# Kernel tuning notes

Measured on AMD Instinct MI355X. Metric: run time of the kernel, lower is better.

The kernel has to match this reference:

```python
import jax, jax.numpy as jnp
import numpy as np

B, N, D, H, MLP = 4, 1024, 1024, 16, 4096  # seq_len N must equal dim D; D = H * dim_head
DH = D // H
EPS = 1e-5


def layernorm(x, g, b):
    mu = jnp.mean(x, axis=-1, keepdims=True)
    var = jnp.var(x, axis=-1, keepdims=True)
    return (x - mu) * jax.lax.rsqrt(var + EPS) * g + b


def setup_inputs() -> dict:
    key = jax.random.key(0)
    ks = jax.random.split(key, 12)
    s = 0.02
    return {
        "x": jax.random.normal(ks[0], (B, N, D), jnp.float32),
        "enc_out": jax.random.normal(ks[1], (B, N, D), jnp.float32),
        # SelfAttention (heads=1, dim_head=D); weights stored (in, out) so we apply x @ W
        "sa_wq": jax.random.normal(ks[2], (D, D), jnp.float32) * s,
        "sa_wk": jax.random.normal(ks[3], (D, D), jnp.float32) * s,
        "sa_wv": jax.random.normal(ks[4], (D, D), jnp.float32) * s,
        "sa_g": jnp.ones((D,), jnp.float32),
        "sa_b": jnp.zeros((D,), jnp.float32),
        # CrossAttention
        "ca_wq": jax.random.normal(ks[5], (D, D), jnp.float32) * s,
        "ca_wk": jax.random.normal(ks[6], (D, D), jnp.float32) * s,
        "ca_wv": jax.random.normal(ks[7], (D, D), jnp.float32) * s,
        "ca_g": jnp.ones((D,), jnp.float32),
        "ca_b": jnp.zeros((D,), jnp.float32),
        # FeedForward
        "w1": jax.random.normal(ks[8], (D, MLP), jnp.float32) * s,
        "b1": jnp.zeros((MLP,), jnp.float32),
        "w2": jax.random.normal(ks[9], (MLP, D), jnp.float32) * s,
        "b2": jnp.zeros((D,), jnp.float32),
        "ff_g": jnp.ones((D,), jnp.float32),
        "ff_b": jnp.zeros((D,), jnp.float32),
    }


def reference(x, enc_out, sa_wq, sa_wk, sa_wv, sa_g, sa_b,
              ca_wq, ca_wk, ca_wv, ca_g, ca_b,
              w1, b1, w2, b2, ff_g, ff_b):
    b, n, d = x.shape
    # --- SelfAttention: heads=1, dim_head=dim -> scale = dim**-0.5 ---
    sa_scale = 1.0 / jnp.sqrt(jnp.asarray(d, x.dtype))
    q = x @ sa_wq
    k = x @ sa_wk
    v = x @ sa_wv
    dots = jnp.einsum('bid,bjd->bij', q, k) * sa_scale
    attn = jax.nn.softmax(dots, axis=-1)
    sa = jnp.einsum('bij,bjd->bid', attn, v)
    sa = layernorm(sa + x, sa_g, sa_b)

    # --- CrossAttention: Q . (K K^T) before softmax ---
    dh = d // H
    ca_scale = 1.0 / jnp.sqrt(jnp.asarray(dh, x.dtype))
    qc = sa @ ca_wq                                     # [b, n, d]; broadcast over heads
    kc = (enc_out @ ca_wk).reshape(b, n, H, dh).transpose(0, 2, 1, 3)  # [b, h, n, dh]
    vc = (enc_out @ ca_wv).reshape(b, n, H, dh).transpose(0, 2, 1, 3)
    kkt = jnp.einsum('bhid,bhjd->bhij', kc, kc) * ca_scale             # [b, h, n, n]
    dots = jnp.einsum('bid,bhjd->bhij', qc, kkt) * ca_scale            # q's d contracts kkt's last dim (n == d)
    attn = jax.nn.softmax(dots, axis=-1)
    out = jnp.einsum('bhij,bhjd->bhid', attn, vc)
    out = out.transpose(0, 2, 1, 3).reshape(b, n, d)
    ca = layernorm(out + enc_out, ca_g, ca_b)

    # --- FeedForward (dropout = identity in eval) ---
    h = jax.nn.gelu(ca @ w1 + b1, approximate=False) @ w2 + b2
    return layernorm(h + ca, ff_g, ff_b)
```

## Files before the change

kernel.cpp:

```cpp
#include <hip/hip_runtime.h>
#include <math.h>
#include <stdint.h>

typedef unsigned short u16;
typedef u16   u16x8 __attribute__((ext_vector_type(8)));
typedef __bf16 bf16x8 __attribute__((ext_vector_type(8)));
typedef float  f32x4 __attribute__((ext_vector_type(4)));

#define B_   4
#define N_   1024
#define D_   1024
#define MLP_ 4096

__device__ __forceinline__ float bf2f(u16 v) {
    unsigned u = ((unsigned)v) << 16;
    return __builtin_bit_cast(float, u);
}
__device__ __forceinline__ u16 f2bf(float f) {
    unsigned u = __builtin_bit_cast(unsigned, f);
    u += 0x7fff + ((u >> 16) & 1);
    return (u16)(u >> 16);
}
__device__ __forceinline__ bf16x8 ld8(const u16* p) {
    return __builtin_bit_cast(bf16x8, *(const u16x8*)p);
}
__device__ __forceinline__ void gll16(const u16* g, u16* l) {
    __builtin_amdgcn_global_load_lds(
        (const __attribute__((address_space(1))) unsigned int*)g,
        (__attribute__((address_space(3))) unsigned int*)l,
        16, 0, 0);
}

__global__ __launch_bounds__(256)
void prep_all(const float* __restrict__ x, const float* __restrict__ enc,
              u16* __restrict__ xB, u16* __restrict__ encB,
              const float* __restrict__ p0, const float* __restrict__ p1,
              const float* __restrict__ p2, const float* __restrict__ p3,
              const float* __restrict__ p4, const float* __restrict__ p5,
              u16* __restrict__ Wsa, u16* __restrict__ Wca)
{
    __shared__ u16 tile[32][33];
    int bid = blockIdx.x;
    if (bid < 4096) {
        const float* in = x; u16* out = xB;
        if (bid >= 2048) { in = enc; out = encB; bid -= 2048; }
        long i = (long)bid * 256 + threadIdx.x;
        f32x4 a = *(const f32x4*)&in[i * 8];
        f32x4 b = *(const f32x4*)&in[i * 8 + 4];
        u16x8 h;
        h[0] = f2bf(a[0]); h[1] = f2bf(a[1]); h[2] = f2bf(a[2]); h[3] = f2bf(a[3]);
        h[4] = f2bf(b[0]); h[5] = f2bf(b[1]); h[6] = f2bf(b[2]); h[7] = f2bf(b[3]);
        *(u16x8*)&out[i * 8] = h;
        return;
    }
    int sub = bid - 4096;
    const int z = sub >> 10;
    const int t2 = sub & 1023;
    const int bx = (t2 & 31) * 32, by = (t2 >> 5) * 32;
    const float* in = p0;
    if (z == 1) in = p1;
    else if (z == 2) in = p2;
    else if (z == 3) in = p3;
    else if (z == 4) in = p4;
    else if (z == 5) in = p5;
    u16* out = (z < 3) ? Wsa + (long)z * (1 << 20) : Wca + (long)(z - 3) * (1 << 20);
    const int tx = threadIdx.x & 31, ty = threadIdx.x >> 5;
#pragma unroll
    for (int i = ty; i < 32; i += 8)
        tile[i][tx] = f2bf(in[(long)(by + i) * 1024 + bx + tx]);
    __syncthreads();
#pragma unroll
    for (int i = ty; i < 32; i += 8)
        out[(long)(bx + i) * 1024 + by + tx] = tile[tx][i];
}

template<int TM, int TN, int SEL, int OUTF32, int BIAS, int GELU>
__global__ __launch_bounds__(256, (TM + TN >= 256) ? 3 : 4)
void gemm_a(const u16* __restrict__ A0, const u16* __restrict__ A1,
            const u16* __restrict__ B0, const u16* __restrict__ B1,
            void* __restrict__ C0v, void* __restrict__ C1v,
            const float* __restrict__ bias,
            float scale, int K,
            int lda, int ldb, int ldc,
            long sA, long sB, long sC)
{
    constexpr int MT = TM / 32, NT = TN / 32;
    __shared__ alignas(16) u16 As[2][TM * 32];
    __shared__ alignas(16) u16 Bs[2][TN * 32];
    int by = blockIdx.y, bz = blockIdx.z;
    const u16* A = A0; const u16* Bt = B0; char* Cp = (char*)C0v;
    if (SEL == 1) {
        int half = gridDim.y >> 1;
        if (by >= half) { A = A1; Bt = B1; Cp = (char*)C1v; by -= half; }
    }
    if (SEL == 2) {
        int half = gridDim.z >> 1;
        if (bz >= half) { A = A1; Bt = B1; Cp = (char*)C1v; bz -= half; }
    }
    A += bz * sA;  Bt += bz * sB;  Cp += bz * sC * (OUTF32 ? 4 : 2);
    const int m0 = blockIdx.x * TM, n0 = by * TN;
    const int t = threadIdx.x, lane = t & 63, w = t >> 6;
    const int wr = (w >> 1) * (TM / 2), wc = (w & 1) * (TN / 2);
    const int fr = lane & 15, fq = lane >> 4, fk = fq * 8;
    f32x4 acc[MT][NT] = {};

    const int r0a = t >> 2, c0a = (t & 3) * 8;
    auto stageA = [&](u16* dst, int k0) {
#pragma unroll
        for (int p = 0; p < TM / 64; p++)
            gll16(A + (long)(m0 + p * 64 + r0a) * lda + k0 + c0a, dst + p * 2048 + w * 512);
    };
    auto stageB = [&](u16* dst, int k0) {
#pragma unroll
        for (int p = 0; p < TN / 64; p++)
            gll16(Bt + (long)(n0 + p * 64 + r0a) * ldb + k0 + c0a, dst + p * 2048 + w * 512);
    };

    stageA(As[0], 0);
    stageB(Bs[0], 0);
    int cur = 0;
    for (int k0 = 0; k0 < K; k0 += 32) {
        __syncthreads();
        if (k0 + 32 < K) {
            stageA(As[cur ^ 1], k0 + 32);
            stageB(Bs[cur ^ 1], k0 + 32);
        }
        const u16* as = As[cur];
        const u16* bs = Bs[cur];
        bf16x8 af[MT], bfv[NT];
#pragma unroll
        for (int mt = 0; mt < MT; mt++) af [mt] = ld8(&as[(wr + mt * 16 + fr) * 32 + fk]);
#pragma unroll
        for (int nt = 0; nt < NT; nt++) bfv[nt] = ld8(&bs[(wc + nt * 16 + fr) * 32 + fk]);
#pragma unroll
        for (int mt = 0; mt < MT; mt++)
#pragma unroll
            for (int nt = 0; nt < NT; nt++)
                acc[mt][nt] = __builtin_amdgcn_mfma_f32_16x16x32_bf16(af[mt], bfv[nt], acc[mt][nt], 0, 0, 0);
        cur ^= 1;
    }

#pragma unroll
    for (int nt = 0; nt < NT; nt++) {
        const int col = n0 + wc + nt * 16 + fr;
        float bv = 0.f;
        if (BIAS) bv = bias[col];
#pragma unroll
        for (int mt = 0; mt < MT; mt++) {
            const int rbase = m0 + wr + mt * 16 + fq * 4;
#pragma unroll
            for (int r = 0; r < 4; r++) {
                float v = acc[mt][nt][r] * scale;
                if (BIAS) v += bv;
                if (GELU) v = 0.5f * v * (1.0f + erff(v * 0.70710678118654752f));
                long idx = (long)(rbase + r) * ldc + col;
                if (OUTF32) ((float*)Cp)[idx] = v;
                else        ((u16*) Cp)[idx] = f2bf(v);
            }
        }
    }
}

template<int INF32>
__global__ __launch_bounds__(256)
void transpose_cast(const void* __restrict__ in, u16* __restrict__ out,
                    int R, int C, long sIn, long sOut)
{
    __shared__ u16 tile[32][33];
    const char* ip = (const char*)in + (long)blockIdx.z * sIn * (INF32 ? 4 : 2);
    u16*        op = out + (long)blockIdx.z * sOut;
    const int bx = blockIdx.x * 32, by = blockIdx.y * 32;
    const int tx = threadIdx.x & 31, ty = threadIdx.x >> 5;
#pragma unroll
    for (int i = ty; i < 32; i += 8) {
        long idx = (long)(by + i) * C + bx + tx;
        tile[i][tx] = INF32 ? f2bf(((const float*)ip)[idx]) : ((const u16*)ip)[idx];
    }
    __syncthreads();
#pragma unroll
    for (int i = ty; i < 32; i += 8) op[(long)(bx + i) * R + by + tx] = tile[tx][i];
}

__global__ __launch_bounds__(256)
void transpose_ff(const float* __restrict__ w1, const float* __restrict__ w2,
                  u16* __restrict__ o1, u16* __restrict__ o2)
{
    __shared__ u16 tile[32][33];
    const float* in; u16* out; int R, C, bx, by;
    if (blockIdx.z == 0) {
        in = w1; out = o1; R = 1024; C = 4096;
        bx = blockIdx.x; by = blockIdx.y;
    } else {
        in = w2; out = o2; R = 4096; C = 1024;
        bx = blockIdx.x >> 2; by = blockIdx.y * 4 + (blockIdx.x & 3);
    }
    const int x0 = bx * 32, y0 = by * 32;
    const int tx = threadIdx.x & 31, ty = threadIdx.x >> 5;
#pragma unroll
    for (int i = ty; i < 32; i += 8)
        tile[i][tx] = f2bf(in[(long)(y0 + i) * C + x0 + tx]);
    __syncthreads();
#pragma unroll
    for (int i = ty; i < 32; i += 8)
        out[(long)(x0 + i) * R + y0 + tx] = tile[tx][i];
}

__global__ __launch_bounds__(256)
void softmax_1024(const float* __restrict__ in, u16* __restrict__ out)
{
    const int lane = threadIdx.x & 63, wv = threadIdx.x >> 6;
    const long row = (long)blockIdx.x * 4 + wv;
    const float* p = in + row * 1024 + lane * 16;
    float v[16];
#pragma unroll
    for (int q = 0; q < 4; q++) {
        f32x4 a = *(const f32x4*)(p + q * 4);
#pragma unroll
        for (int e = 0; e < 4; e++) v[q * 4 + e] = a[e];
    }
    float mx = v[0];
#pragma unroll
    for (int i = 1; i < 16; i++) mx = fmaxf(mx, v[i]);
#pragma unroll
    for (int off = 32; off; off >>= 1) mx = fmaxf(mx, __shfl_xor(mx, off, 64));
    float s = 0.f;
#pragma unroll
    for (int i = 0; i < 16; i++) { v[i] = __expf(v[i] - mx); s += v[i]; }
#pragma unroll
    for (int off = 32; off; off >>= 1) s += __shfl_xor(s, off, 64);
    const float inv = 1.0f / s;
    u16* qp = out + row * 1024 + lane * 16;
#pragma unroll
    for (int q = 0; q < 2; q++) {
        u16x8 o;
#pragma unroll
        for (int e = 0; e < 8; e++) o[e] = f2bf(v[q * 8 + e] * inv);
        *(u16x8*)(qp + q * 8) = o;
    }
}

template<int AF32, int RESF32, int OUTF32>
__global__ __launch_bounds__(256)
void ln_res(const void* __restrict__ Av, const void* __restrict__ Rv,
            const float* __restrict__ g, const float* __restrict__ be,
            void* __restrict__ out)
{
    const int lane = threadIdx.x & 63, wv = threadIdx.x >> 6;
    const long row = (long)blockIdx.x * 4 + wv;
    const long off = row * 1024 + lane * 16;
    const int c0 = lane * 16;
    float v[16];
    if (AF32) {
#pragma unroll
        for (int q = 0; q < 4; q++) {
            f32x4 a = *((const f32x4*)((const float*)Av + off) + q);
#pragma unroll
            for (int e = 0; e < 4; e++) v[q * 4 + e] = a[e];
        }
    } else {
#pragma unroll
        for (int q = 0; q < 2; q++) {
            u16x8 a = *((const u16x8*)((const u16*)Av + off) + q);
#pragma unroll
            for (int e = 0; e < 8; e++) v[q * 8 + e] = bf2f(a[e]);
        }
    }
    if (RESF32) {
#pragma unroll
        for (int q = 0; q < 4; q++) {
            f32x4 a = *((const f32x4*)((const float*)Rv + off) + q);
#pragma unroll
            for (int e = 0; e < 4; e++) v[q * 4 + e] += a[e];
        }
    } else {
#pragma unroll
        for (int q = 0; q < 2; q++) {
            u16x8 a = *((const u16x8*)((const u16*)Rv + off) + q);
#pragma unroll
            for (int e = 0; e < 8; e++) v[q * 8 + e] += bf2f(a[e]);
        }
    }
    float s = 0.f;
#pragma unroll
    for (int i = 0; i < 16; i++) s += v[i];
#pragma unroll
    for (int o = 32; o; o >>= 1) s += __shfl_xor(s, o, 64);
    const float mu = s * (1.f / 1024.f);
    float s2 = 0.f;
#pragma unroll
    for (int i = 0; i < 16; i++) { float d = v[i] - mu; s2 += d * d; }
#pragma unroll
    for (int o = 32; o; o >>= 1) s2 += __shfl_xor(s2, o, 64);
    const float rs = rsqrtf(s2 * (1.f / 1024.f) + 1e-5f);

    float ov[16];
#pragma unroll
    for (int q = 0; q < 4; q++) {
        f32x4 gv = *(const f32x4*)&g[c0 + q * 4];
        f32x4 bv = *(const f32x4*)&be[c0 + q * 4];
#pragma unroll
        for (int e = 0; e < 4; e++)
            ov[q * 4 + e] = (v[q * 4 + e] - mu) * rs * gv[e] + bv[e];
    }
    if (OUTF32) {
#pragma unroll
        for (int q = 0; q < 4; q++) {
            f32x4 o;
#pragma unroll
            for (int e = 0; e < 4; e++) o[e] = ov[q * 4 + e];
            *((f32x4*)((float*)out + off) + q) = o;
        }
    } else {
#pragma unroll
        for (int q = 0; q < 2; q++) {
            u16x8 o;
#pragma unroll
            for (int e = 0; e < 8; e++) o[e] = f2bf(ov[q * 8 + e]);
            *((u16x8*)((u16*)out + off) + q) = o;
        }
    }
}

__global__ __launch_bounds__(256, 3)
void flash_ca(const u16* __restrict__ P, const u16* __restrict__ Kc,
              const u16* __restrict__ VT, u16* __restrict__ O)
{
    __shared__ alignas(16) u16 Ks[2][64 * 64];
    __shared__ alignas(16) u16 Vs[2][64 * 64];
    __shared__ alignas(16) u16 Ps[128 * 72];
    const int b = blockIdx.z, h = blockIdx.y, it = blockIdx.x;
    const long base = (long)b * N_ * D_;
    const int t = threadIdx.x, lane = t & 63, w = t >> 6;
    const int fr = lane & 15, fq = lane >> 4;

    bf16x8 qf[2][2];
#pragma unroll
    for (int mt = 0; mt < 2; mt++)
#pragma unroll
        for (int hf = 0; hf < 2; hf++)
            qf[mt][hf] = ld8(&P[base + (long)(it * 128 + w * 32 + mt * 16 + fr) * D_
                                + h * 64 + hf * 32 + fq * 8]);

    auto stageK = [&](int buf, int jt) {
#pragma unroll
        for (int p = 0; p < 2; p++)
            gll16(Kc + base + (long)(jt * 64 + p * 32 + (t >> 3)) * D_ + h * 64 + (t & 7) * 8,
                  &Ks[buf][p * 2048 + w * 512]);
    };
    auto stageV = [&](int buf, int jt) {
#pragma unroll
        for (int p = 0; p < 2; p++)
            gll16(VT + base + (long)(h * 64 + p * 32 + (t >> 3)) * D_ + jt * 64 + (t & 7) * 8,
                  &Vs[buf][p * 2048 + w * 512]);
    };

    f32x4 o[2][4] = {};
    float l_lane[2][4] = {};

    stageK(0, 0); stageV(0, 0);
    int cur = 0;
    for (int jt = 0; jt < 16; jt++) {
        __syncthreads();
        if (jt + 1 < 16) { stageK(cur ^ 1, jt + 1); stageV(cur ^ 1, jt + 1); }
        const u16* ks = Ks[cur];
        const u16* vs = Vs[cur];

        f32x4 st[2][4] = {};
        __builtin_amdgcn_s_setprio(1);
#pragma unroll
        for (int nt = 0; nt < 4; nt++) {
            bf16x8 b0 = ld8(&ks[(nt * 16 + fr) * 64 + fq * 8]);
            bf16x8 b1 = ld8(&ks[(nt * 16 + fr) * 64 + 32 + fq * 8]);
#pragma unroll
            for (int mt = 0; mt < 2; mt++) {
                st[mt][nt] = __builtin_amdgcn_mfma_f32_16x16x32_bf16(qf[mt][0], b0, st[mt][nt], 0, 0, 0);
                st[mt][nt] = __builtin_amdgcn_mfma_f32_16x16x32_bf16(qf[mt][1], b1, st[mt][nt], 0, 0, 0);
            }
        }
        __builtin_amdgcn_s_setprio(0);
#pragma unroll
        for (int mt = 0; mt < 2; mt++)
#pragma unroll
            for (int nt = 0; nt < 4; nt++)
#pragma unroll
                for (int r = 0; r < 4; r++) {
                    float e = __expf(st[mt][nt][r]);
                    l_lane[mt][r] += e;
                    Ps[(w * 32 + mt * 16 + fq * 4 + r) * 72 + nt * 16 + fr] = f2bf(e);
                }
        __asm__ volatile("s_waitcnt lgkmcnt(0)" ::: "memory");
        bf16x8 vf[4][2];
#pragma unroll
        for (int dt = 0; dt < 4; dt++) {
            vf[dt][0] = ld8(&vs[(dt * 16 + fr) * 64 + fq * 8]);
            vf[dt][1] = ld8(&vs[(dt * 16 + fr) * 64 + 32 + fq * 8]);
        }
        __builtin_amdgcn_s_setprio(1);
#pragma unroll
        for (int mt = 0; mt < 2; mt++) {
            bf16x8 p0 = ld8(&Ps[(w * 32 + mt * 16 + fr) * 72 + fq * 8]);
            bf16x8 p1 = ld8(&Ps[(w * 32 + mt * 16 + fr) * 72 + 32 + fq * 8]);
#pragma unroll
            for (int dt = 0; dt < 4; dt++) {
                o[mt][dt] = __builtin_amdgcn_mfma_f32_16x16x32_bf16(p0, vf[dt][0], o[mt][dt], 0, 0, 0);
                o[mt][dt] = __builtin_amdgcn_mfma_f32_16x16x32_bf16(p1, vf[dt][1], o[mt][dt], 0, 0, 0);
            }
        }
        __builtin_amdgcn_s_setprio(0);
        cur ^= 1;
    }
#pragma unroll
    for (int mt = 0; mt < 2; mt++)
#pragma unroll
        for (int r = 0; r < 4; r++) {
            float lt = l_lane[mt][r];
#pragma unroll
            for (int off = 1; off < 16; off <<= 1) lt += __shfl_xor(lt, off, 64);
            l_lane[mt][r] = 1.0f / lt;
        }
#pragma unroll
    for (int mt = 0; mt < 2; mt++)
#pragma unroll
        for (int dt = 0; dt < 4; dt++)
#pragma unroll
            for (int r = 0; r < 4; r++)
                O[base + (long)(it * 128 + w * 32 + mt * 16 + fq * 4 + r) * D_
                  + h * 64 + dt * 16 + fr] = f2bf(o[mt][dt][r] * l_lane[mt][r]);
}

extern "C" void kernel_launch(void* const* d_in, const int* in_sizes, int n_in,
                              void* d_out, int out_size, void* d_ws, size_t ws_size,
                              hipStream_t stream)
{
    const float* x     = (const float*)d_in[0];
    const float* enc   = (const float*)d_in[1];
    const float* sa_wq = (const float*)d_in[2];
    const float* sa_wk = (const float*)d_in[3];
    const float* sa_wv = (const float*)d_in[4];
    const float* sa_g  = (const float*)d_in[5];
    const float* sa_b  = (const float*)d_in[6];
    const float* ca_wq = (const float*)d_in[7];
    const float* ca_wk = (const float*)d_in[8];
    const float* ca_wv = (const float*)d_in[9];
    const float* ca_g  = (const float*)d_in[10];
    const float* ca_b  = (const float*)d_in[11];
    const float* w1    = (const float*)d_in[12];
    const float* b1    = (const float*)d_in[13];
    const float* w2    = (const float*)d_in[14];
    const float* b2    = (const float*)d_in[15];
    const float* ff_g  = (const float*)d_in[16];
    const float* ff_b  = (const float*)d_in[17];

    char* ws = (char*)d_ws;
    const size_t MB = 1ull << 20;
    u16*  xB    = (u16*)(ws + 0 * MB);
    u16*  attnB = (u16*)(ws + 0 * MB);
    u16*  w2T   = (u16*)(ws + 0 * MB);
    u16*  encB  = (u16*)(ws + 8 * MB);
    u16*  w1T   = (u16*)(ws + 8 * MB);
    u16*  Wsa   = (u16*)(ws + 16 * MB);
    u16*  Wca   = (u16*)(ws + 22 * MB);
    float* h2F  = (float*)(ws + 16 * MB);
    u16*  qBsa  = (u16*)(ws + 28 * MB);
    u16*  E     = (u16*)(ws + 28 * MB);
    u16*  kBsa  = (u16*)(ws + 36 * MB);
    u16*  qBca  = (u16*)(ws + 36 * MB);
    u16*  calnB = (u16*)(ws + 36 * MB);
    u16*  vTB   = (u16*)(ws + 44 * MB);
    u16*  kBca  = (u16*)(ws + 44 * MB);
    u16*  h1B   = (u16*)(ws + 44 * MB);
    u16*  vcTB  = (u16*)(ws + 52 * MB);
    float* scF  = (float*)(ws + 60 * MB);
    u16*  kcT   = (u16*)(ws + 60 * MB);

    const dim3 blk(256, 1, 1);
    const long M1 = (long)N_ * D_;
    const long W1M = (long)1024 * 1024;

    prep_all<<<dim3(10240, 1, 1), blk, 0, stream>>>(
        x, enc, xB, encB, sa_wq, sa_wk, sa_wv, ca_wq, ca_wk, ca_wv, Wsa, Wca);

    gemm_a<128,128,1,0,0,0><<<dim3(32, 16, 1), blk, 0, stream>>>(
        xB, xB, Wsa, Wsa + W1M, qBsa, kBsa, nullptr,
        1.f, 1024, 1024, 1024, 1024, 0, 0, 0);
    gemm_a<128,128,2,0,0,0><<<dim3(8, 8, 8), blk, 0, stream>>>(
        Wsa + 2 * W1M, Wca + 2 * W1M, xB, encB, vTB, vcTB, nullptr,
        1.f, 1024, 1024, 1024, 1024, 0, M1, M1);
    gemm_a<128,64,0,1,0,0><<<dim3(8, 16, 4), blk, 0, stream>>>(
        qBsa, nullptr, kBsa, nullptr, scF, nullptr, nullptr,
        0.03125f, 1024, 1024, 1024, 1024, M1, M1, M1);
    softmax_1024<<<dim3(1024, 1, 1), blk, 0, stream>>>(scF, attnB);
    gemm_a<128,64,0,1,0,0><<<dim3(8, 16, 4), blk, 0, stream>>>(
        attnB, nullptr, vTB, nullptr, scF, nullptr, nullptr,
        1.f, 1024, 1024, 1024, 1024, M1, M1, M1);
    ln_res<1,1,0><<<dim3(1024, 1, 1), blk, 0, stream>>>(scF, x, sa_g, sa_b, E);

    gemm_a<128,128,1,0,0,0><<<dim3(32, 16, 1), blk, 0, stream>>>(
        E, encB, Wca, Wca + W1M, qBca, kBca, nullptr,
        1.f, 1024, 1024, 1024, 1024, 0, 0, 0);
    transpose_cast<0><<<dim3(32, 32, 4), blk, 0, stream>>>(kBca, kcT, 1024, 1024, M1, M1);
    gemm_a<128,64,0,0,0,0><<<dim3(8, 16, 4), blk, 0, stream>>>(
        qBca, nullptr, kcT, nullptr, attnB, nullptr, nullptr,
        0.015625f, 1024, 1024, 1024, 1024, M1, M1, M1);
    flash_ca<<<dim3(8, 16, 4), blk, 0, stream>>>(attnB, kBca, vcTB, E);
    ln_res<0,1,0><<<dim3(1024, 1, 1), blk, 0, stream>>>(E, enc, ca_g, ca_b, calnB);

    transpose_ff<<<dim3(128, 32, 2), blk, 0, stream>>>(w1, w2, w1T, w2T);
    gemm_a<128,128,0,0,1,1><<<dim3(32, 32, 1), blk, 0, stream>>>(
        calnB, nullptr, w1T, nullptr, h1B, nullptr, b1,
        1.f, 1024, 1024, 1024, 4096, 0, 0, 0);
    gemm_a<128,64,0,1,1,0><<<dim3(32, 16, 1), blk, 0, stream>>>(
        h1B, nullptr, w2T, nullptr, h2F, nullptr, b2,
        1.f, 4096, 4096, 4096, 1024, 0, 0, 0);
    ln_res<1,0,1><<<dim3(1024, 1, 1), blk, 0, stream>>>(h2F, calnB, ff_g, ff_b, (float*)d_out);
}
```

Measured before the change: 517.9 us.

## Merge QKV/V-transpose GEMMs into one launch and add BK=64 K-tiles

Factors the GEMM mainloop into a device body with a configurable K-tile depth (BK), and uses BK=64 for several attention, projection and FF2 GEMMs. This halves the number of barriers and K iterations per tile. It also merges the Q/K projection GEMM and the two V-transpose GEMMs into a single 1024-block launch, cutting one launch and improving wave fill. The larger LDS footprint lowers the occupancy hint from 3/4 to 2/3 blocks per CU, so fewer blocks can hide latency.

```diff
diff --git a/kernel.cpp b/kernel.cpp
--- a/kernel.cpp
+++ b/kernel.cpp
@@ -74,69 +74,58 @@
         out[(long)(bx + i) * 1024 + by + tx] = tile[tx][i];
 }
 
-template<int TM, int TN, int SEL, int OUTF32, int BIAS, int GELU>
-__global__ __launch_bounds__(256, (TM + TN >= 256) ? 3 : 4)
-void gemm_a(const u16* __restrict__ A0, const u16* __restrict__ A1,
-            const u16* __restrict__ B0, const u16* __restrict__ B1,
-            void* __restrict__ C0v, void* __restrict__ C1v,
-            const float* __restrict__ bias,
-            float scale, int K,
-            int lda, int ldb, int ldc,
-            long sA, long sB, long sC)
+template<int TM, int TN, int BK, int OUTF32, int BIAS, int GELU>
+__device__ __forceinline__ void gemm_body(
+    const u16* __restrict__ A, const u16* __restrict__ Bt, char* __restrict__ Cp,
+    const float* __restrict__ bias, float scale, int K,
+    int lda, int ldb, int ldc, int m0, int n0)
 {
     constexpr int MT = TM / 32, NT = TN / 32;
-    __shared__ alignas(16) u16 As[2][TM * 32];
-    __shared__ alignas(16) u16 Bs[2][TN * 32];
-    int by = blockIdx.y, bz = blockIdx.z;
-    const u16* A = A0; const u16* Bt = B0; char* Cp = (char*)C0v;
-    if (SEL == 1) {
-        int half = gridDim.y >> 1;
-        if (by >= half) { A = A1; Bt = B1; Cp = (char*)C1v; by -= half; }
-    }
-    if (SEL == 2) {
-        int half = gridDim.z >> 1;
-        if (bz >= half) { A = A1; Bt = B1; Cp = (char*)C1v; bz -= half; }
-    }
-    A += bz * sA;  Bt += bz * sB;  Cp += bz * sC * (OUTF32 ? 4 : 2);
-    const int m0 = blockIdx.x * TM, n0 = by * TN;
+    constexpr int CPT = BK / 8;
+    constexpr int RPP = 2048 / BK;
+    __shared__ alignas(16) u16 As[2][TM * BK];
+    __shared__ alignas(16) u16 Bs[2][TN * BK];
     const int t = threadIdx.x, lane = t & 63, w = t >> 6;
     const int wr = (w >> 1) * (TM / 2), wc = (w & 1) * (TN / 2);
     const int fr = lane & 15, fq = lane >> 4, fk = fq * 8;
     f32x4 acc[MT][NT] = {};
 
-    const int r0a = t >> 2, c0a = (t & 3) * 8;
+    const int r0a = t / CPT, c0a = (t % CPT) * 8;
     auto stageA = [&](u16* dst, int k0) {
 #pragma unroll
-        for (int p = 0; p < TM / 64; p++)
-            gll16(A + (long)(m0 + p * 64 + r0a) * lda + k0 + c0a, dst + p * 2048 + w * 512);
+        for (int p = 0; p < TM / RPP; p++)
+            gll16(A + (long)(m0 + p * RPP + r0a) * lda + k0 + c0a, dst + p * 2048 + w * 512);
     };
     auto stageB = [&](u16* dst, int k0) {
 #pragma unroll
-        for (int p = 0; p < TN / 64; p++)
-            gll16(Bt + (long)(n0 + p * 64 + r0a) * ldb + k0 + c0a, dst + p * 2048 + w * 512);
+        for (int p = 0; p < TN / RPP; p++)
+            gll16(Bt + (long)(n0 + p * RPP + r0a) * ldb + k0 + c0a, dst + p * 2048 + w * 512);
     };
 
     stageA(As[0], 0);
     stageB(Bs[0], 0);
     int cur = 0;
-    for (int k0 = 0; k0 < K; k0 += 32) {
+    for (int k0 = 0; k0 < K; k0 += BK) {
         __syncthreads();
-        if (k0 + 32 < K) {
-            stageA(As[cur ^ 1], k0 + 32);
-            stageB(Bs[cur ^ 1], k0 + 32);
+        if (k0 + BK < K) {
+            stageA(As[cur ^ 1], k0 + BK);
+            stageB(Bs[cur ^ 1], k0 + BK);
         }
         const u16* as = As[cur];
         const u16* bs = Bs[cur];
-        bf16x8 af[MT], bfv[NT];
-#pragma unroll
-        for (int mt = 0; mt < MT; mt++) af [mt] = ld8(&as[(wr + mt * 16 + fr) * 32 + fk]);
-#pragma unroll
-        for (int nt = 0; nt < NT; nt++) bfv[nt] = ld8(&bs[(wc + nt * 16 + fr) * 32 + fk]);
-#pragma unroll
-        for (int mt = 0; mt < MT; mt++)
-#pragma unroll
-            for (int nt = 0; nt < NT; nt++)
-                acc[mt][nt] = __builtin_amdgcn_mfma_f32_16x16x32_bf16(af[mt], bfv[nt], acc[mt][nt], 0, 0, 0);
+#pragma unroll
+        for (int kk = 0; kk < BK; kk += 32) {
+            bf16x8 af[MT], bfv[NT];
+#pragma unroll
+            for (int mt = 0; mt < MT; mt++) af [mt] = ld8(&as[(wr + mt * 16 + fr) * BK + kk + fk]);
+#pragma unroll
+            for (int nt = 0; nt < NT; nt++) bfv[nt] = ld8(&bs[(wc + nt * 16 + fr) * BK + kk + fk]);
+#pragma unroll
+            for (int mt = 0; mt < MT; mt++)
+#pragma unroll
+                for (int nt = 0; nt < NT; nt++)
+                    acc[mt][nt] = __builtin_amdgcn_mfma_f32_16x16x32_bf16(af[mt], bfv[nt], acc[mt][nt], 0, 0, 0);
+        }
         cur ^= 1;
     }
 
@@ -159,6 +148,55 @@
             }
         }
     }
+}
+
+template<int TM, int TN, int BK, int SEL, int OUTF32, int BIAS, int GELU>
+__global__ __launch_bounds__(256, ((TM + TN >= 256) ? ((BK == 64) ? 2 : 3)
+                                                    : ((BK == 64) ? 3 : 4)))
+void gemm_a(const u16* __restrict__ A0, const u16* __restrict__ A1,
+            const u16* __restrict__ B0, const u16* __restrict__ B1,
+            void* __restrict__ C0v, void* __restrict__ C1v,
+            const float* __restrict__ bias,
+            float scale, int K,
+            int lda, int ldb, int ldc,
+            long sA, long sB, long sC)
+{
+    int by = blockIdx.y, bz = blockIdx.z;
+    const u16* A = A0; const u16* Bt = B0; char* Cp = (char*)C0v;
+    if (SEL == 1) {
+        int half = gridDim.y >> 1;
+        if (by >= half) { A = A1; Bt = B1; Cp = (char*)C1v; by -= half; }
+    }
+    A += bz * sA;  Bt += bz * sB;  Cp += bz * sC * (OUTF32 ? 4 : 2);
+    gemm_body<TM, TN, BK, OUTF32, BIAS, GELU>(
+        A, Bt, Cp, bias, scale, K, lda, ldb, ldc, blockIdx.x * TM, by * TN);
+}
+
+__global__ __launch_bounds__(256, 3)
+void gemm_qkv4(const u16* __restrict__ xB,  const u16* __restrict__ Wq,
+               const u16* __restrict__ Wk,  u16* __restrict__ qB,
+               u16* __restrict__ kB,
+               const u16* __restrict__ Wv,  const u16* __restrict__ Wvc,
+               const u16* __restrict__ encB,
+               u16* __restrict__ vTB, u16* __restrict__ vcTB)
+{
+    const long M1 = (long)N_ * D_;
+    int bid = blockIdx.x;
+    const u16* A; const u16* Bt; u16* C; int m0, n0;
+    if (bid < 512) {
+        int bx = bid & 31, by = bid >> 5;
+        A = xB; m0 = bx * 128;
+        if (by < 8) { Bt = Wq; C = qB; n0 = by * 128; }
+        else        { Bt = Wk; C = kB; n0 = (by - 8) * 128; }
+    } else {
+        int sub = bid - 512;
+        int bx = sub & 7, by = (sub >> 3) & 7, bz = sub >> 6;
+        m0 = bx * 128; n0 = by * 128;
+        if (bz < 4) { A = Wv;  Bt = xB   + (long)bz * M1;       C = vTB  + (long)bz * M1; }
+        else        { A = Wvc; Bt = encB + (long)(bz - 4) * M1; C = vcTB + (long)(bz - 4) * M1; }
+    }
+    gemm_body<128, 128, 32, 0, 0, 0>(
+        A, Bt, (char*)C, nullptr, 1.f, 1024, 1024, 1024, 1024, m0, n0);
 }
 
 template<int INF32>
@@ -480,36 +518,33 @@
     prep_all<<<dim3(10240, 1, 1), blk, 0, stream>>>(
         x, enc, xB, encB, sa_wq, sa_wk, sa_wv, ca_wq, ca_wk, ca_wv, Wsa, Wca);
 
-    gemm_a<128,128,1,0,0,0><<<dim3(32, 16, 1), blk, 0, stream>>>(
-        xB, xB, Wsa, Wsa + W1M, qBsa, kBsa, nullptr,
-        1.f, 1024, 1024, 1024, 1024, 0, 0, 0);
-    gemm_a<128,128,2,0,0,0><<<dim3(8, 8, 8), blk, 0, stream>>>(
-        Wsa + 2 * W1M, Wca + 2 * W1M, xB, encB, vTB, vcTB, nullptr,
-        1.f, 1024, 1024, 1024, 1024, 0, M1, M1);
-    gemm_a<128,64,0,1,0,0><<<dim3(8, 16, 4), blk, 0, stream>>>(
+    gemm_qkv4<<<dim3(1024, 1, 1), blk, 0, stream>>>(
+        xB, Wsa, Wsa + W1M, qBsa, kBsa,
+        Wsa + 2 * W1M, Wca + 2 * W1M, encB, vTB, vcTB);
+    gemm_a<128,64,64,0,1,0,0><<<dim3(8, 16, 4), blk, 0, stream>>>(
         qBsa, nullptr, kBsa, nullptr, scF, nullptr, nullptr,
         0.03125f, 1024, 1024, 1024, 1024, M1, M1, M1);
     softmax_1024<<<dim3(1024, 1, 1), blk, 0, stream>>>(scF, attnB);
-    gemm_a<128,64,0,1,0,0><<<dim3(8, 16, 4), blk, 0, stream>>>(
+    gemm_a<128,64,64,0,1,0,0><<<dim3(8, 16, 4), blk, 0, stream>>>(
         attnB, nullptr, vTB, nullptr, scF, nullptr, nullptr,
         1.f, 1024, 1024, 1024, 1024, M1, M1, M1);
     ln_res<1,1,0><<<dim3(1024, 1, 1), blk, 0, stream>>>(scF, x, sa_g, sa_b, E);
 
-    gemm_a<128,128,1,0,0,0><<<dim3(32, 16, 1), blk, 0, stream>>>(
+    gemm_a<128,128,64,1,0,0,0><<<dim3(32, 16, 1), blk, 0, stream>>>(
         E, encB, Wca, Wca + W1M, qBca, kBca, nullptr,
         1.f, 1024, 1024, 1024, 1024, 0, 0, 0);
     transpose_cast<0><<<dim3(32, 32, 4), blk, 0, stream>>>(kBca, kcT, 1024, 1024, M1, M1);
-    gemm_a<128,64,0,0,0,0><<<dim3(8, 16, 4), blk, 0, stream>>>(
+    gemm_a<128,64,64,0,0,0,0><<<dim3(8, 16, 4), blk, 0, stream>>>(
         qBca, nullptr, kcT, nullptr, attnB, nullptr, nullptr,
         0.015625f, 1024, 1024, 1024, 1024, M1, M1, M1);
     flash_ca<<<dim3(8, 16, 4), blk, 0, stream>>>(attnB, kBca, vcTB, E);
     ln_res<0,1,0><<<dim3(1024, 1, 1), blk, 0, stream>>>(E, enc, ca_g, ca_b, calnB);
 
     transpose_ff<<<dim3(128, 32, 2), blk, 0, stream>>>(w1, w2, w1T, w2T);
-    gemm_a<128,128,0,0,1,1><<<dim3(32, 32, 1), blk, 0, stream>>>(
+    gemm_a<128,128,32,0,0,1,1><<<dim3(32, 32, 1), blk, 0, stream>>>(
         calnB, nullptr, w1T, nullptr, h1B, nullptr, b1,
         1.f, 1024, 1024, 1024, 4096, 0, 0, 0);
-    gemm_a<128,64,0,1,1,0><<<dim3(32, 16, 1), blk, 0, stream>>>(
+    gemm_a<128,64,64,0,1,1,0><<<dim3(32, 16, 1), blk, 0, stream>>>(
         h1B, nullptr, w2T, nullptr, h2F, nullptr, b2,
         1.f, 4096, 4096, 4096, 1024, 0, 0, 0);
     ln_res<1,0,1><<<dim3(1024, 1, 1), blk, 0, stream>>>(h2F, calnB, ff_g, ff_b, (float*)d_out);
```

Result: faster. 503.3 us (-2.8%).
